# Kernel tuning notes

Measured on AMD Instinct MI355X. Metric: run time of the kernel, lower is better.

## Reference

```python
import jax, jax.numpy as jnp
import numpy as np

# --- model dims ---
N = 360        # nodes
B = 8          # batch
T = 7500       # hidden_steps = tr/dt = 750/0.1
RATIO = 10     # dt_ratio = dtt/dt
HEMO = T // RATIO
INPUT = 2
DMAX = 500

# --- FastDMFParams defaults ---
DT = 0.1
SQRT_DT = DT ** 0.5
DTT_S = 1.0 / 1000.0            # dtt / 1000 (seconds)
W_E, W_I, I_0 = 1.0, 0.7, 0.382
TAU_E, TAU_I = 100.0, 10.0
GAMMA_E, GAMMA_I = 0.641 / 1000.0, 1.0 / 1000.0
SIGMA_E, SIGMA_I = 0.005, 0.005
AE, BE, DE = 310.0, 125.0, 0.16
AI, BI, DI = 615.0, 177.0, 0.087
G, JN = 2.0, 0.15
G_EE = 1.4
ITAU_S, ITAU_F, ITAU_0 = 1.0 / 0.65, 1.0 / 0.41, 1.0 / 0.98
IALPHA, RHO = 1.0 / 0.32, 0.34
K1, K2, K3 = 2.38, 2.0, 0.48
V0 = 0.2


def setup_inputs() -> dict:
    key = jax.random.key(0)
    k1, k2, k3, k4 = jax.random.split(key, 4)
    baseline = jnp.array([0.0, 0.0, 0.0, 1.0, 1.0, 1.0], jnp.float32).reshape(1, 6, 1)
    state = 0.45 * jax.random.uniform(k1, (N, 6, B), jnp.float32) + baseline
    delays = jnp.zeros((N, DMAX, B), jnp.float32)  # unused (use_delay_based=False)
    noise_in = jax.random.normal(k2, (N, T, INPUT, B), jnp.float32)
    noise_out = jax.random.normal(k3, (N, B), jnp.float32)
    sc = jax.random.uniform(k4, (B, N, N), jnp.float32) / N  # normalized structural connectivity
    return {"state": state, "delays": delays, "noise_in": noise_in,
            "noise_out": noise_out, "sc": sc}


def _firing_rate(a, b, d, cur):
    x = a * cur - b
    return x / (1.0 - jnp.exp(-d * x) + 1e-8)


def _simulate(state, noise_in, noise_out, sc):
    E, I = state[:, 0, :], state[:, 1, :]          # (N,B)
    s, f = state[:, 2, :], state[:, 3, :]
    v, q = state[:, 4, :], state[:, 5, :]

    # inhibitory gain (non-scalar branch): Ji = 1 + 0.75*g*rowsum(sc), (N,B)
    Ji = (1.0 + 0.75 * G * jnp.sum(sc, axis=-1)).T

    # (N,T,INPUT,B) -> (HEMO, RATIO, N, INPUT, B)
    noise = jnp.transpose(noise_in, (1, 0, 2, 3)).reshape(HEMO, RATIO, N, INPUT, B)

    def neural_step(carry, nz):
        E, I = carry
        En, In = nz[:, 0, :], nz[:, 1, :]
        conn = jnp.einsum('bnm,mb->nb', sc, E)                 # delayed-coupling surrogate
        I_E = jax.nn.relu(W_E * I_0 + G_EE * JN * E + G * JN * conn - Ji * I)
        I_I = jax.nn.relu(W_I * I_0 + JN * E - I)
        R_E = _firing_rate(AE, BE, DE, I_E)
        R_I = _firing_rate(AI, BI, DI, I_I)
        dE = -E / TAU_E + (1.0 - E) * GAMMA_E * R_E
        dI = -I / TAU_I + GAMMA_I * R_I
        E = jax.nn.relu(E + DT * dE + SIGMA_E * En * SQRT_DT)
        I = jax.nn.relu(I + DT * dI + SIGMA_I * In * SQRT_DT)
        return (E, I), None

    def hemo_step(carry, noise_block):
        E, I, s, f, v, q = carry
        (E, I), _ = jax.lax.scan(neural_step, (E, I), noise_block)
        # Balloon-Windkessel Euler step at dtt (seconds)
        v_ia = v ** IALPHA
        ds = E - ITAU_S * s - ITAU_F * (f - 1.0)
        df = s
        dv = (f - v_ia) * ITAU_0
        dq = (f / RHO * (1.0 - (1.0 - RHO) ** (1.0 / f)) - q * v_ia / v) * ITAU_0
        s = s + DTT_S * ds
        f = f + DTT_S * df
        v = v + DTT_S * dv
        q = q + DTT_S * dq
        return (E, I, s, f, v, q), None

    (E, I, s, f, v, q), _ = jax.lax.scan(hemo_step, (E, I, s, f, v, q), noise)
    bold = 100.0 * V0 * (K1 * (1.0 - q) + K2 * (1.0 - q / v) + K3 * (1.0 - v)) + noise_out
    next_state = jnp.stack([E, I, s, f, v, q], axis=1)  # (N,6,B)
    return next_state, bold


def reference(state, delays, noise_in, noise_out, sc):
    # delays buffer unused (params.use_delay_based = False)
    return _simulate(state, noise_in, noise_out, sc)
```

## Files before the change

kernel.cpp:

```cpp
#include <hip/hip_runtime.h>


typedef unsigned int u32;
typedef uint4 u32x4;

#define NN 360
#define NB 8
#define NT 7500
#define NHEMO 750

#define S_SC 45720.0f
#define S_E  64.0f
#define CONN_K 1.0252653e-7f

#if __has_builtin(__builtin_amdgcn_sdot4)
#define DOT4(a,b,c) __builtin_amdgcn_sdot4((a),(b),(c),false)
#elif __has_builtin(__builtin_amdgcn_udot4)
#define DOT4(a,b,c) (int)__builtin_amdgcn_udot4((u32)(a),(u32)(b),(u32)(c),false)
#else
static __device__ __forceinline__ int DOT4(int a, int b, int c) {
  #pragma unroll
  for (int i = 0; i < 4; ++i) c += ((a >> (8*i)) & 0xff) * ((b >> (8*i)) & 0xff);
  return c;
}
#endif

__device__ __forceinline__ float frcp(float x) {
#if __has_builtin(__builtin_amdgcn_rcpf)
  return __builtin_amdgcn_rcpf(x);
#else
  return 1.0f / x;
#endif
}
__device__ __forceinline__ float fexp2(float x) {
#if __has_builtin(__builtin_amdgcn_exp2f)
  return __builtin_amdgcn_exp2f(x);
#else
  return exp2f(x);
#endif
}
__device__ __forceinline__ float flog2(float x) {
#if __has_builtin(__builtin_amdgcn_logf)
  return __builtin_amdgcn_logf(x);
#else
  return log2f(x);
#endif
}

template <int CTRL>
__device__ __forceinline__ int dpp_add_i(int x) {
  return x + __builtin_amdgcn_mov_dpp(x, CTRL, 0xF, 0xF, true);
}
template <int CTRL>
__device__ __forceinline__ float dpp_add_f(float x) {
  return x + __int_as_float(__builtin_amdgcn_mov_dpp(__float_as_int(x), CTRL, 0xF, 0xF, true));
}

__global__ __launch_bounds__(512, 2) void dmf_kernel(
    const float* __restrict__ state,
    const float* __restrict__ noise_in,
    const float* __restrict__ noise_out,
    const float* __restrict__ sc,
    float* __restrict__ out)
{
  const int b   = blockIdx.x;
  const int tid = threadIdx.x;
  const int w   = tid >> 6;
  const int l   = tid & 63;
  const int cg  = l & 3;
  const int rg  = l >> 2;

  const bool upd = (cg < 3) && (rg < 15);
  const int lrow = 3*rg + cg;
  const int urow = 45*w + lrow;

  __shared__ u32 Eq[2][96];

  if (tid < 192) ((u32*)Eq)[tid] = 0;

  int scp[3][24];
  float rs[3] = {0.f, 0.f, 0.f};
  const int c0 = 90 * cg;
  #pragma unroll
  for (int j = 0; j < 3; ++j) {
    const int rr = 3*rg + j;
    const bool rvalid = (rr < 45);
    const float* sp = sc + ((size_t)b*NN + (45*w + rr))*NN;
    #pragma unroll
    for (int k = 0; k < 24; ++k) {
      int pack = 0;
      #pragma unroll
      for (int e = 0; e < 4; ++e) {
        const int cc = 4*k + e;
        int q = 0;
        if (rvalid && cc < 90) {
          const float x = sp[c0 + cc];
          rs[j] += x;
          q = (int)rintf(x * S_SC);
        }
        pack |= q << (8*e);
      }
      scp[j][k] = pack;
    }
  }

  #pragma unroll
  for (int j = 0; j < 3; ++j) {
    rs[j] = dpp_add_f<0xB1>(rs[j]);
    rs[j] = dpp_add_f<0x4E>(rs[j]);
  }
  const float rsum = (cg == 0) ? rs[0] : ((cg == 1) ? rs[1] : rs[2]);

  float E=0.f, I=0.f, ss=0.f, ff=0.f, vv=0.f, qq=0.f, Ji=0.f;
  const float* np = noise_in + (size_t)urow * NT * 2 * NB + b;
  float n0E=0.f, n0I=0.f, n1E=0.f, n1I=0.f;
  int boff = 0;
  __syncthreads();
  if (upd) {
    Ji = 1.0f + 1.5f * rsum;
    const float* st = state + (size_t)urow * 6 * NB + b;
    E  = st[0];
    I  = st[NB];
    ss = st[2*NB];
    ff = st[3*NB];
    vv = st[4*NB];
    qq = st[5*NB];
    const int ch = urow / 90;
    boff = urow + 6*ch;
    int q = (int)rintf(E * S_E);
    q = q > 127 ? 127 : q;
    ((char*)&Eq[0][0])[boff] = (char)q;
    n0E = np[0];      n0I = np[NB];
    n1E = np[2*NB];   n1I = np[3*NB];
  }
  np += 4*NB;
  __syncthreads();

  const u32x4* eq0 = (const u32x4*)&Eq[0][24*cg];
  const u32x4* eq1 = (const u32x4*)&Eq[1][24*cg];
  char* pb0 = (char*)&Eq[0][0] + boff;
  char* pb1 = (char*)&Eq[1][0] + boff;

  auto body = [&](const u32x4* cur, char* nxt, bool PF, bool hemo) {
    u32x4 ev[6];
    #pragma unroll
    for (int kk = 0; kk < 6; ++kk) ev[kk] = cur[kk];

    float n2E = n1E, n2I = n1I;
    if (PF) {
      if (upd) { n2E = np[0]; n2I = np[NB]; }
      np += 2*NB;
    }

    int a0 = 0, a1 = 0, a2 = 0;
    #pragma unroll
    for (int kk = 0; kk < 6; ++kk) {
      const u32x4 e = ev[kk];
      a0 = DOT4(scp[0][4*kk+0], (int)e.x, a0);
      a1 = DOT4(scp[1][4*kk+0], (int)e.x, a1);
      a2 = DOT4(scp[2][4*kk+0], (int)e.x, a2);
      a0 = DOT4(scp[0][4*kk+1], (int)e.y, a0);
      a1 = DOT4(scp[1][4*kk+1], (int)e.y, a1);
      a2 = DOT4(scp[2][4*kk+1], (int)e.y, a2);
      a0 = DOT4(scp[0][4*kk+2], (int)e.z, a0);
      a1 = DOT4(scp[1][4*kk+2], (int)e.z, a1);
      a2 = DOT4(scp[2][4*kk+2], (int)e.z, a2);
      a0 = DOT4(scp[0][4*kk+3], (int)e.w, a0);
      a1 = DOT4(scp[1][4*kk+3], (int)e.w, a1);
      a2 = DOT4(scp[2][4*kk+3], (int)e.w, a2);
    }
    a0 = dpp_add_i<0xB1>(a0); a0 = dpp_add_i<0x4E>(a0);
    a1 = dpp_add_i<0xB1>(a1); a1 = dpp_add_i<0x4E>(a1);
    a2 = dpp_add_i<0xB1>(a2); a2 = dpp_add_i<0x4E>(a2);
    const int ci = (cg == 0) ? a0 : ((cg == 1) ? a1 : a2);

    if (upd) {
      const float cs = (float)ci * CONN_K;
      float I_E = fmaxf(0.382f + 0.21f*E + cs - Ji*I, 0.f);
      float I_I = fmaxf(0.2674f + 0.15f*E - I, 0.f);
      const float xE  = 310.f*I_E - 125.f;
      const float R_E = xE * frcp(1.f - __expf(-0.16f*xE) + 1e-8f);
      const float xI  = 615.f*I_I - 177.f;
      const float R_I = xI * frcp(1.f - __expf(-0.087f*xI) + 1e-8f);
      const float dE = -E*0.01f + (1.f - E)*0.000641f*R_E;
      const float dI = -I*0.1f  + 0.001f*R_I;
      E = fmaxf(E + 0.1f*dE + 0.00158113883f*n0E, 0.f);
      I = fmaxf(I + 0.1f*dI + 0.00158113883f*n0I, 0.f);
      int q = (int)rintf(E * S_E);
      q = q > 127 ? 127 : q;
      *nxt = (char)q;
      if (hemo) {
        const float l2v  = flog2(vv);
        const float v_ia = fexp2(3.125f * l2v);
        const float v_r  = fexp2(2.125f * l2v);
        const float ds_  = E - 1.53846153846f*ss - 2.43902439024f*(ff - 1.f);
        const float df_  = ss;
        const float dv_  = (ff - v_ia) * 1.02040816327f;
        const float pw   = fexp2(-0.59946207f * frcp(ff));
        const float dq_  = (ff*2.94117647059f*(1.f - pw) - qq*v_r) * 1.02040816327f;
        ss += 1e-3f*ds_;
        ff += 1e-3f*df_;
        vv += 1e-3f*dv_;
        qq += 1e-3f*dq_;
      }
    }
    n0E = n1E; n0I = n1I;
    n1E = n2E; n1I = n2I;
    __syncthreads();
  };

  for (int hs = 0; hs < NHEMO; ++hs) {
    body(eq0, pb1, true, false);
    body(eq1, pb0, true, false);
    body(eq0, pb1, true, false);
    body(eq1, pb0, true, false);
    body(eq0, pb1, true, false);
    body(eq1, pb0, true, false);
    body(eq0, pb1, true, false);
    body(eq1, pb0, true, false);
    if (hs != NHEMO - 1) {
      body(eq0, pb1, true, false);
      body(eq1, pb0, true, true);
    } else {
      body(eq0, pb1, false, false);
      body(eq1, pb0, false, true);
    }
  }

  if (upd) {
    float* o = out + (size_t)urow * 6 * NB + b;
    o[0]    = E;
    o[NB]   = I;
    o[2*NB] = ss;
    o[3*NB] = ff;
    o[4*NB] = vv;
    o[5*NB] = qq;
    out[NN*6*NB + urow*NB + b] =
        20.f*(2.38f*(1.f - qq) + 2.f*(1.f - qq/vv) + 0.48f*(1.f - vv))
        + noise_out[urow*NB + b];
  }
}

extern "C" void kernel_launch(void* const* d_in, const int* in_sizes, int n_in,
                              void* d_out, int out_size, void* d_ws, size_t ws_size,
                              hipStream_t stream) {
  const float* state     = (const float*)d_in[0];
  const float* noise_in  = (const float*)d_in[2];
  const float* noise_out = (const float*)d_in[3];
  const float* sc        = (const float*)d_in[4];
  float* out = (float*)d_out;
  dmf_kernel<<<NB, 512, 0, stream>>>(state, noise_in, noise_out, sc, out);
}
```

Measured before the change: 4.676 ms.

## Use lighter LDS-only barrier, split dot accumulators, fold exp scaling constants

Replaces __syncthreads with a custom barrier that waits only on LDS counters (lgkmcnt), so in-flight global noise prefetches no longer stall each step. It also splits the int8 dot-product chain into two independent accumulators to shorten the dependency chain. It replaces __expf with a direct exp2 using pre-folded constants, and rintf with add-0.5 truncation. Risks: the barrier leaves global loads outstanding across steps, and the rounding differs slightly for ties, though E stays non-negative.

```diff
diff --git a/kernel.cpp b/kernel.cpp
--- a/kernel.cpp
+++ b/kernel.cpp
@@ -54,6 +54,14 @@
 template <int CTRL>
 __device__ __forceinline__ float dpp_add_f(float x) {
   return x + __int_as_float(__builtin_amdgcn_mov_dpp(__float_as_int(x), CTRL, 0xF, 0xF, true));
+}
+
+__device__ __forceinline__ void lds_barrier() {
+  __builtin_amdgcn_sched_barrier(0);
+  asm volatile("s_waitcnt lgkmcnt(0)" ::: "memory");
+  __builtin_amdgcn_s_barrier();
+  asm volatile("" ::: "memory");
+  __builtin_amdgcn_sched_barrier(0);
 }
 
 __global__ __launch_bounds__(512, 2) void dmf_kernel(
@@ -152,9 +160,9 @@
       np += 2*NB;
     }
 
-    int a0 = 0, a1 = 0, a2 = 0;
-    #pragma unroll
-    for (int kk = 0; kk < 6; ++kk) {
+    int a0 = 0, a1 = 0, a2 = 0, b0 = 0, b1 = 0, b2 = 0;
+    #pragma unroll
+    for (int kk = 0; kk < 3; ++kk) {
       const u32x4 e = ev[kk];
       a0 = DOT4(scp[0][4*kk+0], (int)e.x, a0);
       a1 = DOT4(scp[1][4*kk+0], (int)e.x, a1);
@@ -169,6 +177,23 @@
       a1 = DOT4(scp[1][4*kk+3], (int)e.w, a1);
       a2 = DOT4(scp[2][4*kk+3], (int)e.w, a2);
     }
+    #pragma unroll
+    for (int kk = 3; kk < 6; ++kk) {
+      const u32x4 e = ev[kk];
+      b0 = DOT4(scp[0][4*kk+0], (int)e.x, b0);
+      b1 = DOT4(scp[1][4*kk+0], (int)e.x, b1);
+      b2 = DOT4(scp[2][4*kk+0], (int)e.x, b2);
+      b0 = DOT4(scp[0][4*kk+1], (int)e.y, b0);
+      b1 = DOT4(scp[1][4*kk+1], (int)e.y, b1);
+      b2 = DOT4(scp[2][4*kk+1], (int)e.y, b2);
+      b0 = DOT4(scp[0][4*kk+2], (int)e.z, b0);
+      b1 = DOT4(scp[1][4*kk+2], (int)e.z, b1);
+      b2 = DOT4(scp[2][4*kk+2], (int)e.z, b2);
+      b0 = DOT4(scp[0][4*kk+3], (int)e.w, b0);
+      b1 = DOT4(scp[1][4*kk+3], (int)e.w, b1);
+      b2 = DOT4(scp[2][4*kk+3], (int)e.w, b2);
+    }
+    a0 += b0; a1 += b1; a2 += b2;
     a0 = dpp_add_i<0xB1>(a0); a0 = dpp_add_i<0x4E>(a0);
     a1 = dpp_add_i<0xB1>(a1); a1 = dpp_add_i<0x4E>(a1);
     a2 = dpp_add_i<0xB1>(a2); a2 = dpp_add_i<0x4E>(a2);
@@ -179,14 +204,14 @@
       float I_E = fmaxf(0.382f + 0.21f*E + cs - Ji*I, 0.f);
       float I_I = fmaxf(0.2674f + 0.15f*E - I, 0.f);
       const float xE  = 310.f*I_E - 125.f;
-      const float R_E = xE * frcp(1.f - __expf(-0.16f*xE) + 1e-8f);
+      const float R_E = xE * frcp(1.f - fexp2(-0.23083120f*xE) + 1e-8f);
       const float xI  = 615.f*I_I - 177.f;
-      const float R_I = xI * frcp(1.f - __expf(-0.087f*xI) + 1e-8f);
+      const float R_I = xI * frcp(1.f - fexp2(-0.12551447f*xI) + 1e-8f);
       const float dE = -E*0.01f + (1.f - E)*0.000641f*R_E;
       const float dI = -I*0.1f  + 0.001f*R_I;
       E = fmaxf(E + 0.1f*dE + 0.00158113883f*n0E, 0.f);
       I = fmaxf(I + 0.1f*dI + 0.00158113883f*n0I, 0.f);
-      int q = (int)rintf(E * S_E);
+      int q = (int)(E * S_E + 0.5f);
       q = q > 127 ? 127 : q;
       *nxt = (char)q;
       if (hemo) {
@@ -206,7 +231,7 @@
     }
     n0E = n1E; n0I = n1I;
     n1E = n2E; n1I = n2I;
-    __syncthreads();
+    lds_barrier();
   };
 
   for (int hs = 0; hs < NHEMO; ++hs) {
```

Measured after the change: 4.734 ms. About the same (+1.2%).
